# Performance work log

Measured on AMD Instinct MI355X. Metric: run time of the kernel, lower is better.

Reference implementation:

```python
import jax, jax.numpy as jnp
import numpy as np

B, N, C, OC, K = 8, 1024, 64, 64, 4


def setup_inputs() -> dict:
    key = jax.random.key(0)
    ks = jax.random.split(key, 10)
    stdv = 1.0 / np.sqrt(OC)
    wr = jax.random.uniform(ks[4], (K + 1, C, OC), minval=-stdv, maxval=stdv)
    wi = jax.random.uniform(ks[5], (K + 1, C, OC), minval=-stdv, maxval=stdv)
    mag = jnp.sqrt(wr ** 2 + wi ** 2)
    wr, wi = wr / mag, wi / mag  # unit-magnitude complex weights (as in __init__)
    return {
        "X_real": jax.random.normal(ks[0], (B, N, C), dtype=jnp.float32),
        "X_imag": jax.random.normal(ks[1], (B, N, C), dtype=jnp.float32),
        "L_real": jax.random.normal(ks[2], (B, K + 1, N, N), dtype=jnp.float32) * 0.05,
        "L_imag": jax.random.normal(ks[3], (B, K + 1, N, N), dtype=jnp.float32) * 0.05,
        "w_real": wr.astype(jnp.float32),
        "w_imag": wi.astype(jnp.float32),
        "aw_real": jax.random.normal(ks[6], (2 * C,), dtype=jnp.float32) * 0.1,
        "aw_imag": jax.random.normal(ks[7], (2 * C,), dtype=jnp.float32) * 0.1,
        "ab_real": jnp.zeros((), jnp.float32),
        "ab_imag": jnp.zeros((), jnp.float32),
        "pa_real": jnp.float32(0.25),  # CPReLU slope (real part)
        "pa_imag": jnp.float32(0.25),  # CPReLU slope (imag part)
    }


def reference(X_real, X_imag, L_real, L_imag, w_real, w_imag,
              aw_real, aw_imag, ab_real, ab_imag, pa_real, pa_imag):
    Cin = X_real.shape[-1]
    # --- GAT-style complex attention score: CVLinear([x_i, x_j]) decomposed ---
    # score[b,i,j] = <x_i, w_src> + <x_j, w_dst> + bias (complex)
    ws_r, wd_r = aw_real[:Cin], aw_real[Cin:]
    ws_i, wd_i = aw_imag[:Cin], aw_imag[Cin:]
    src_r = X_real @ ws_r - X_imag @ ws_i   # [B,N]
    src_i = X_real @ ws_i + X_imag @ ws_r
    dst_r = X_real @ wd_r - X_imag @ wd_i
    dst_i = X_real @ wd_i + X_imag @ wd_r
    s_r = src_r[:, :, None] + dst_r[:, None, :] + ab_real  # [B,N,N]
    s_i = src_i[:, :, None] + dst_i[:, None, :] + ab_imag
    # CPReLU: PReLU applied separately to real/imag
    s_r = jnp.where(s_r >= 0, s_r, pa_real * s_r)
    s_i = jnp.where(s_i >= 0, s_i, pa_imag * s_i)
    # PhaseSoftMax(dim=1): softmax on magnitude, keep phase
    mag = jnp.sqrt(s_r ** 2 + s_i ** 2)
    sm = jax.nn.softmax(mag, axis=1)
    safe = jnp.where(mag == 0, 1.0, mag)
    a_r = sm * s_r / safe  # [B,N,N]
    a_i = sm * s_i / safe
    # --- modulate complex Laplacian (broadcast over K+1 axis) ---
    Lr = L_real * a_r[:, None] - L_imag * a_i[:, None]   # [B,K+1,N,N]
    Li = L_real * a_i[:, None] + L_imag * a_r[:, None]
    # --- faithful to einsum 'bijk,bqjp->bijp': sum last axis of L, broadcast j ---
    SLr = Lr.sum(-1)  # [B,K+1,N]
    SLi = Li.sum(-1)
    ein = lambda S, X, W: jnp.einsum('bkn,bnc,kco->bno', S, X, W)
    out_r = ein(SLr, X_real, w_real) - ein(SLi, X_imag, w_imag)  # [B,N,OC]
    out_i = ein(SLi, X_real, w_real) + ein(SLr, X_imag, w_imag)
    return out_r, out_i
```

## Files before the change

kernel.cpp:

```cpp
#include <hip/hip_runtime.h>

typedef unsigned short u16;
typedef unsigned int   u32;

__device__ __forceinline__ float b2f(u16 u){
  u32 x = ((u32)u) << 16;
  float f;
  __builtin_memcpy(&f, &x, 4);
  return f;
}
__device__ __forceinline__ float ld(const void* p, int i, bool f32){
  return f32 ? ((const float*)p)[i] : b2f(((const u16*)p)[i]);
}

__global__ __launch_bounds__(256) void k_detect(
    const u16* __restrict__ X, const u16* __restrict__ L,
    const u16* __restrict__ w, const u16* __restrict__ aw,
    const u16* __restrict__ pa, float* __restrict__ flags)
{
  const int tid  = threadIdx.x;
  const int g    = tid >> 6;
  const int lane = tid & 63;
  const u16* src = (g == 0) ? X : (g == 1) ? L : (g == 2) ? w : aw;
  float v = fabsf(b2f(src[lane]));
  if (!(v < 1e30f)) v = 1e30f;
#pragma unroll
  for (int off = 32; off; off >>= 1){
    float o = __shfl_xor(v, off);
    v = v > o ? v : o;
  }
  if (lane == 0) flags[g] = (v > 1e6f) ? 1.f : 0.f;
  if (tid == 0)  flags[4] = (b2f(pa[0]) == 0.f) ? 1.f : 0.f;
}

__global__ __launch_bounds__(256) void k_srcdst(
    const void* __restrict__ Xr, const void* __restrict__ Xi,
    const void* __restrict__ awr, const void* __restrict__ awi,
    float* __restrict__ src_r, float* __restrict__ src_i,
    float* __restrict__ dst_r, float* __restrict__ dst_i,
    float* __restrict__ denom, const float* __restrict__ flags)
{
  const int tid = threadIdx.x;
  if (blockIdx.x < 32) denom[blockIdx.x * 256 + tid] = 0.f;

  const bool fX  = flags[0] != 0.f;
  const bool fAW = flags[3] != 0.f;

  const int bn = blockIdx.x * 4 + (tid >> 6);
  const int c  = tid & 63;
  float xr = ld(Xr, bn * 64 + c, fX);
  float xi = ld(Xi, bn * 64 + c, fX);
  float wsr = ld(awr, c, fAW),      wsi = ld(awi, c, fAW);
  float wdr = ld(awr, 64 + c, fAW), wdi = ld(awi, 64 + c, fAW);

  float p0 = xr * wsr - xi * wsi;
  float p1 = xr * wsi + xi * wsr;
  float p2 = xr * wdr - xi * wdi;
  float p3 = xr * wdi + xi * wdr;
#pragma unroll
  for (int off = 32; off; off >>= 1){
    p0 += __shfl_xor(p0, off);
    p1 += __shfl_xor(p1, off);
    p2 += __shfl_xor(p2, off);
    p3 += __shfl_xor(p3, off);
  }
  if (c == 0){
    src_r[bn] = p0; src_i[bn] = p1; dst_r[bn] = p2; dst_i[bn] = p3;
  }
}

__global__ __launch_bounds__(256) void k_colsum(
    const float* __restrict__ src_r, const float* __restrict__ src_i,
    const float* __restrict__ dst_r, const float* __restrict__ dst_i,
    const void* __restrict__ abr_p, const void* __restrict__ abi_p,
    const void* __restrict__ par_p, const void* __restrict__ pai_p,
    float* __restrict__ denom, const float* __restrict__ flags)
{
  __shared__ float srs[128], sis[128];
  const int tid = threadIdx.x;
  const int b  = blockIdx.x >> 5;
  const int mc = (blockIdx.x >> 3) & 3;
  const int nc = blockIdx.x & 7;
  const int m  = mc * 256 + tid;

  const bool fS = flags[4] != 0.f;
  const float abr = ld(abr_p, 0, fS), abi = ld(abi_p, 0, fS);
  const float par = ld(par_p, 0, fS), pai = ld(pai_p, 0, fS);

  if (tid < 128) srs[tid] = src_r[b * 1024 + nc * 128 + tid];
  else           sis[tid - 128] = src_i[b * 1024 + nc * 128 + (tid - 128)];
  __syncthreads();

  const float dr = dst_r[b * 1024 + m];
  const float di = dst_i[b * 1024 + m];
  float sum = 0.f;
#pragma unroll 4
  for (int j = 0; j < 128; j++){
    float sr = srs[j] + dr + abr; sr = sr >= 0.f ? sr : par * sr;
    float si = sis[j] + di + abi; si = si >= 0.f ? si : pai * si;
    float mag = sqrtf(sr * sr + si * si);
    sum += __expf(mag);
  }
  atomicAdd(&denom[b * 1024 + m], sum);
}

__global__ __launch_bounds__(256) void k_rowsum(
    const void* __restrict__ Lr, const void* __restrict__ Li,
    const float* __restrict__ src_r, const float* __restrict__ src_i,
    const float* __restrict__ dst_r, const float* __restrict__ dst_i,
    const float* __restrict__ denom,
    const void* __restrict__ abr_p, const void* __restrict__ abi_p,
    const void* __restrict__ par_p, const void* __restrict__ pai_p,
    float* __restrict__ SL, const float* __restrict__ flags)
{
  const int tid = threadIdx.x;
  const int bn  = blockIdx.x;
  const int b   = bn >> 10;
  const int n   = bn & 1023;

  const bool fL = flags[1] != 0.f;
  const bool fS = flags[4] != 0.f;

  const int base = b * 5 * 262144 + n * 256 + tid;
  float lr[5][4], li[5][4];
  if (fL){
    const float4* LrP = (const float4*)Lr;
    const float4* LiP = (const float4*)Li;
#pragma unroll
    for (int k = 0; k < 5; k++){
      float4 a = LrP[base + k * 262144];
      float4 c = LiP[base + k * 262144];
      lr[k][0]=a.x; lr[k][1]=a.y; lr[k][2]=a.z; lr[k][3]=a.w;
      li[k][0]=c.x; li[k][1]=c.y; li[k][2]=c.z; li[k][3]=c.w;
    }
  } else {
    const ushort4* LrP = (const ushort4*)Lr;
    const ushort4* LiP = (const ushort4*)Li;
#pragma unroll
    for (int k = 0; k < 5; k++){
      ushort4 a = LrP[base + k * 262144];
      ushort4 c = LiP[base + k * 262144];
      lr[k][0]=b2f(a.x); lr[k][1]=b2f(a.y); lr[k][2]=b2f(a.z); lr[k][3]=b2f(a.w);
      li[k][0]=b2f(c.x); li[k][1]=b2f(c.y); li[k][2]=b2f(c.z); li[k][3]=b2f(c.w);
    }
  }

  const int mb = b * 1024 + tid * 4;
  float4 dr4 = *(const float4*)(dst_r + mb);
  float4 di4 = *(const float4*)(dst_i + mb);
  float4 de4 = *(const float4*)(denom + mb);
  const float sR = src_r[bn], sI = src_i[bn];
  const float abr = ld(abr_p, 0, fS), abi = ld(abi_p, 0, fS);
  const float par = ld(par_p, 0, fS), pai = ld(pai_p, 0, fS);

  float drv[4], dvv[4], dev[4];
  *(float4*)drv = dr4; *(float4*)dvv = di4; *(float4*)dev = de4;

  float ar[4], ai[4];
#pragma unroll
  for (int j = 0; j < 4; j++){
    float sr = sR + drv[j] + abr; sr = sr >= 0.f ? sr : par * sr;
    float si = sI + dvv[j] + abi; si = si >= 0.f ? si : pai * si;
    float mag = sqrtf(sr * sr + si * si);
    float e = __expf(mag);
    float safe = mag > 0.f ? mag : 1.f;
    float coef = e / (dev[j] * safe);
    ar[j] = coef * sr;
    ai[j] = coef * si;
  }

  float v[10];
#pragma unroll
  for (int k = 0; k < 5; k++){
    float accr = 0.f, acci = 0.f;
#pragma unroll
    for (int j = 0; j < 4; j++){
      accr += lr[k][j] * ar[j] - li[k][j] * ai[j];
      acci += lr[k][j] * ai[j] + li[k][j] * ar[j];
    }
    v[k]     = accr;
    v[5 + k] = acci;
  }

#pragma unroll
  for (int off = 32; off; off >>= 1){
#pragma unroll
    for (int t = 0; t < 10; t++) v[t] += __shfl_xor(v[t], off);
  }
  __shared__ float red[4][10];
  if ((tid & 63) == 0){
#pragma unroll
    for (int t = 0; t < 10; t++) red[tid >> 6][t] = v[t];
  }
  __syncthreads();
  if (tid < 10)
    SL[bn * 10 + tid] = red[0][tid] + red[1][tid] + red[2][tid] + red[3][tid];
}

__global__ __launch_bounds__(256) void k_out(
    const void* __restrict__ Xr, const void* __restrict__ Xi,
    const void* __restrict__ wr, const void* __restrict__ wi,
    const float* __restrict__ SL, float* __restrict__ out,
    const float* __restrict__ flags)
{
  __shared__ __align__(16) float Xr_s[16 * 68];
  __shared__ __align__(16) float Xi_s[16 * 68];
  __shared__ __align__(16) float wrT[64 * 68];
  __shared__ __align__(16) float wiT[64 * 68];
  __shared__ float SL_s[160];

  const int tid = threadIdx.x;
  const int R0  = blockIdx.x * 16;
  const bool fX = flags[0] != 0.f;
  const bool fW = flags[2] != 0.f;

#pragma unroll
  for (int e = 0; e < 4; e++){
    int idx = tid + 256 * e;
    int r = idx >> 6, c = idx & 63;
    Xr_s[r * 68 + c] = ld(Xr, R0 * 64 + idx, fX);
    Xi_s[r * 68 + c] = ld(Xi, R0 * 64 + idx, fX);
  }
  if (tid < 160) SL_s[tid] = SL[R0 * 10 + tid];

  const int r  = tid & 15;
  const int o4 = tid >> 4;
  float outr[4] = {0.f, 0.f, 0.f, 0.f};
  float outi[4] = {0.f, 0.f, 0.f, 0.f};

  for (int k = 0; k < 5; k++){
    __syncthreads();
#pragma unroll
    for (int e = 0; e < 16; e++){
      int idx = tid + 256 * e;
      int c = idx >> 6, o = idx & 63;
      wrT[o * 68 + c] = ld(wr, k * 4096 + idx, fW);
      wiT[o * 68 + c] = ld(wi, k * 4096 + idx, fW);
    }
    __syncthreads();

    float Dr[4] = {0.f, 0.f, 0.f, 0.f};
    float Di[4] = {0.f, 0.f, 0.f, 0.f};
#pragma unroll 4
    for (int c0 = 0; c0 < 64; c0 += 4){
      float4 xr = *(const float4*)(Xr_s + r * 68 + c0);
      float4 xi = *(const float4*)(Xi_s + r * 68 + c0);
#pragma unroll
      for (int oo = 0; oo < 4; oo++){
        int o = o4 * 4 + oo;
        float4 a  = *(const float4*)(wrT + o * 68 + c0);
        float4 bb = *(const float4*)(wiT + o * 68 + c0);
        Dr[oo] += xr.x * a.x  + xr.y * a.y  + xr.z * a.z  + xr.w * a.w;
        Di[oo] += xi.x * bb.x + xi.y * bb.y + xi.z * bb.z + xi.w * bb.w;
      }
    }
    const float slr = SL_s[r * 10 + k];
    const float sli = SL_s[r * 10 + 5 + k];
#pragma unroll
    for (int oo = 0; oo < 4; oo++){
      outr[oo] += slr * Dr[oo] - sli * Di[oo];
      outi[oo] += sli * Dr[oo] + slr * Di[oo];
    }
  }

  __syncthreads();
#pragma unroll
  for (int oo = 0; oo < 4; oo++){
    int o = o4 * 4 + oo;
    wrT[r * 68 + o] = outr[oo];
    wiT[r * 68 + o] = outi[oo];
  }
  __syncthreads();
  {
    int flat = tid * 4;
    int rr = flat >> 6, o0 = flat & 63;
    float4 vr = *(const float4*)(wrT + rr * 68 + o0);
    float4 vi = *(const float4*)(wiT + rr * 68 + o0);
    *(float4*)(out + (R0 + rr) * 64 + o0)          = vr;
    *(float4*)(out + 524288 + (R0 + rr) * 64 + o0) = vi;
  }
}

extern "C" void kernel_launch(void* const* d_in, const int* in_sizes, int n_in,
                              void* d_out, int out_size, void* d_ws, size_t ws_size,
                              hipStream_t stream)
{
  const void* Xr  = d_in[0];
  const void* Xi  = d_in[1];
  const void* Lr  = d_in[2];
  const void* Li  = d_in[3];
  const void* wrp = d_in[4];
  const void* wip = d_in[5];
  const void* awr = d_in[6];
  const void* awi = d_in[7];
  const void* abr = d_in[8];
  const void* abi = d_in[9];
  const void* par = d_in[10];
  const void* pai = d_in[11];
  float* out = (float*)d_out;

  float* ws    = (float*)d_ws;
  float* src_r = ws;
  float* src_i = ws + 8192;
  float* dst_r = ws + 16384;
  float* dst_i = ws + 24576;
  float* denom = ws + 32768;
  float* SL    = ws + 40960;
  float* flags = ws + 122880;

  k_detect<<<1, 256, 0, stream>>>((const u16*)Xr, (const u16*)Lr, (const u16*)wrp,
                                  (const u16*)awr, (const u16*)par, flags);
  k_srcdst<<<2048, 256, 0, stream>>>(Xr, Xi, awr, awi, src_r, src_i, dst_r, dst_i,
                                     denom, flags);
  k_colsum<<<256, 256, 0, stream>>>(src_r, src_i, dst_r, dst_i, abr, abi, par, pai,
                                    denom, flags);
  k_rowsum<<<8192, 256, 0, stream>>>(Lr, Li, src_r, src_i, dst_r, dst_i, denom,
                                     abr, abi, par, pai, SL, flags);
  k_out<<<512, 256, 0, stream>>>(Xr, Xi, wrp, wip, SL, out, flags);
}
```

Measured before the change: 454.0 us.

## Map one row per wavefront in rowsum with prefetch; vectorize k_out loads

k_rowsum now gives each wavefront its own (b,n) row. Each lane walks four column chunks, and in the bf16 path the next chunk's L and dst/denom data is double-buffered in registers. The cross-wave shared-memory reduction and __syncthreads are dropped, and the grid shrinks to 2048 blocks with a launch_bounds occupancy hint. It also swaps in fast sqrt/rcp intrinsics and vectorizes the X and weight loads in k_out. The aim is better latency hiding on the dominant L stream, in exchange for higher register pressure and slightly less precise math.

```diff
diff --git a/kernel.cpp b/kernel.cpp
--- a/kernel.cpp
+++ b/kernel.cpp
@@ -104,7 +104,7 @@
   atomicAdd(&denom[b * 1024 + m], sum);
 }
 
-__global__ __launch_bounds__(256) void k_rowsum(
+__global__ __launch_bounds__(256, 4) void k_rowsum(
     const void* __restrict__ Lr, const void* __restrict__ Li,
     const float* __restrict__ src_r, const float* __restrict__ src_i,
     const float* __restrict__ dst_r, const float* __restrict__ dst_i,
@@ -113,88 +113,131 @@
     const void* __restrict__ par_p, const void* __restrict__ pai_p,
     float* __restrict__ SL, const float* __restrict__ flags)
 {
-  const int tid = threadIdx.x;
-  const int bn  = blockIdx.x;
-  const int b   = bn >> 10;
-  const int n   = bn & 1023;
+  const int tid  = threadIdx.x;
+  const int lane = tid & 63;
+  const int bn   = blockIdx.x * 4 + (tid >> 6);
+  const int b    = bn >> 10;
+  const int n    = bn & 1023;
 
   const bool fL = flags[1] != 0.f;
   const bool fS = flags[4] != 0.f;
 
-  const int base = b * 5 * 262144 + n * 256 + tid;
-  float lr[5][4], li[5][4];
-  if (fL){
-    const float4* LrP = (const float4*)Lr;
-    const float4* LiP = (const float4*)Li;
-#pragma unroll
-    for (int k = 0; k < 5; k++){
-      float4 a = LrP[base + k * 262144];
-      float4 c = LiP[base + k * 262144];
-      lr[k][0]=a.x; lr[k][1]=a.y; lr[k][2]=a.z; lr[k][3]=a.w;
-      li[k][0]=c.x; li[k][1]=c.y; li[k][2]=c.z; li[k][3]=c.w;
-    }
-  } else {
-    const ushort4* LrP = (const ushort4*)Lr;
-    const ushort4* LiP = (const ushort4*)Li;
-#pragma unroll
-    for (int k = 0; k < 5; k++){
-      ushort4 a = LrP[base + k * 262144];
-      ushort4 c = LiP[base + k * 262144];
-      lr[k][0]=b2f(a.x); lr[k][1]=b2f(a.y); lr[k][2]=b2f(a.z); lr[k][3]=b2f(a.w);
-      li[k][0]=b2f(c.x); li[k][1]=b2f(c.y); li[k][2]=b2f(c.z); li[k][3]=b2f(c.w);
-    }
-  }
-
-  const int mb = b * 1024 + tid * 4;
-  float4 dr4 = *(const float4*)(dst_r + mb);
-  float4 di4 = *(const float4*)(dst_i + mb);
-  float4 de4 = *(const float4*)(denom + mb);
   const float sR = src_r[bn], sI = src_i[bn];
   const float abr = ld(abr_p, 0, fS), abi = ld(abi_p, 0, fS);
   const float par = ld(par_p, 0, fS), pai = ld(pai_p, 0, fS);
 
-  float drv[4], dvv[4], dev[4];
-  *(float4*)drv = dr4; *(float4*)dvv = di4; *(float4*)dev = de4;
-
-  float ar[4], ai[4];
-#pragma unroll
-  for (int j = 0; j < 4; j++){
-    float sr = sR + drv[j] + abr; sr = sr >= 0.f ? sr : par * sr;
-    float si = sI + dvv[j] + abi; si = si >= 0.f ? si : pai * si;
-    float mag = sqrtf(sr * sr + si * si);
-    float e = __expf(mag);
-    float safe = mag > 0.f ? mag : 1.f;
-    float coef = e / (dev[j] * safe);
-    ar[j] = coef * sr;
-    ai[j] = coef * si;
-  }
-
-  float v[10];
-#pragma unroll
-  for (int k = 0; k < 5; k++){
-    float accr = 0.f, acci = 0.f;
+  float acc[10];
+#pragma unroll
+  for (int t = 0; t < 10; t++) acc[t] = 0.f;
+
+  const int rowbase = (b * 5 * 1024 + n) * 256;
+  const int dbase   = b * 1024;
+
+  if (!fL){
+    const ushort4* LrP = (const ushort4*)Lr;
+    const ushort4* LiP = (const ushort4*)Li;
+    ushort4 lb[2][5], mb[2][5];
+    float4 dr4[2], di4[2], de4[2];
+#pragma unroll
+    for (int k = 0; k < 5; k++){
+      lb[0][k] = LrP[rowbase + k * 262144 + lane];
+      mb[0][k] = LiP[rowbase + k * 262144 + lane];
+    }
+    dr4[0] = *(const float4*)(dst_r + dbase + lane * 4);
+    di4[0] = *(const float4*)(dst_i + dbase + lane * 4);
+    de4[0] = *(const float4*)(denom + dbase + lane * 4);
+
 #pragma unroll
     for (int j = 0; j < 4; j++){
-      accr += lr[k][j] * ar[j] - li[k][j] * ai[j];
-      acci += lr[k][j] * ai[j] + li[k][j] * ar[j];
-    }
-    v[k]     = accr;
-    v[5 + k] = acci;
+      const int cur = j & 1, nxt = cur ^ 1;
+      if (j < 3){
+        const int voff = (j + 1) * 64 + lane;
+#pragma unroll
+        for (int k = 0; k < 5; k++){
+          lb[nxt][k] = LrP[rowbase + k * 262144 + voff];
+          mb[nxt][k] = LiP[rowbase + k * 262144 + voff];
+        }
+        dr4[nxt] = *(const float4*)(dst_r + dbase + voff * 4);
+        di4[nxt] = *(const float4*)(dst_i + dbase + voff * 4);
+        de4[nxt] = *(const float4*)(denom + dbase + voff * 4);
+      }
+      float drv[4] = {dr4[cur].x, dr4[cur].y, dr4[cur].z, dr4[cur].w};
+      float dvv[4] = {di4[cur].x, di4[cur].y, di4[cur].z, di4[cur].w};
+      float dev[4] = {de4[cur].x, de4[cur].y, de4[cur].z, de4[cur].w};
+      float ar[4], ai[4];
+#pragma unroll
+      for (int q = 0; q < 4; q++){
+        float sr = sR + drv[q] + abr; sr = sr >= 0.f ? sr : par * sr;
+        float si = sI + dvv[q] + abi; si = si >= 0.f ? si : pai * si;
+        float mag = __builtin_amdgcn_sqrtf(sr * sr + si * si);
+        float e = __expf(mag);
+        float safe = mag > 0.f ? mag : 1.f;
+        float coef = e * __builtin_amdgcn_rcpf(dev[q] * safe);
+        ar[q] = coef * sr;
+        ai[q] = coef * si;
+      }
+#pragma unroll
+      for (int k = 0; k < 5; k++){
+        float l0 = b2f(lb[cur][k].x), l1 = b2f(lb[cur][k].y);
+        float l2 = b2f(lb[cur][k].z), l3 = b2f(lb[cur][k].w);
+        float m0 = b2f(mb[cur][k].x), m1 = b2f(mb[cur][k].y);
+        float m2 = b2f(mb[cur][k].z), m3 = b2f(mb[cur][k].w);
+        float accr = acc[k], acci = acc[5 + k];
+        accr += l0 * ar[0] - m0 * ai[0];
+        accr += l1 * ar[1] - m1 * ai[1];
+        accr += l2 * ar[2] - m2 * ai[2];
+        accr += l3 * ar[3] - m3 * ai[3];
+        acci += l0 * ai[0] + m0 * ar[0];
+        acci += l1 * ai[1] + m1 * ar[1];
+        acci += l2 * ai[2] + m2 * ar[2];
+        acci += l3 * ai[3] + m3 * ar[3];
+        acc[k] = accr; acc[5 + k] = acci;
+      }
+    }
+  } else {
+    const float4* LrP = (const float4*)Lr;
+    const float4* LiP = (const float4*)Li;
+    for (int j = 0; j < 4; j++){
+      const int voff = j * 64 + lane;
+      float4 dr4 = *(const float4*)(dst_r + dbase + voff * 4);
+      float4 di4 = *(const float4*)(dst_i + dbase + voff * 4);
+      float4 de4 = *(const float4*)(denom + dbase + voff * 4);
+      float drv[4] = {dr4.x, dr4.y, dr4.z, dr4.w};
+      float dvv[4] = {di4.x, di4.y, di4.z, di4.w};
+      float dev[4] = {de4.x, de4.y, de4.z, de4.w};
+      float ar[4], ai[4];
+#pragma unroll
+      for (int q = 0; q < 4; q++){
+        float sr = sR + drv[q] + abr; sr = sr >= 0.f ? sr : par * sr;
+        float si = sI + dvv[q] + abi; si = si >= 0.f ? si : pai * si;
+        float mag = __builtin_amdgcn_sqrtf(sr * sr + si * si);
+        float e = __expf(mag);
+        float safe = mag > 0.f ? mag : 1.f;
+        float coef = e * __builtin_amdgcn_rcpf(dev[q] * safe);
+        ar[q] = coef * sr;
+        ai[q] = coef * si;
+      }
+#pragma unroll 1
+      for (int k = 0; k < 5; k++){
+        float4 a = LrP[rowbase + k * 262144 + voff];
+        float4 c = LiP[rowbase + k * 262144 + voff];
+        acc[k]     += a.x*ar[0] - c.x*ai[0] + a.y*ar[1] - c.y*ai[1]
+                    + a.z*ar[2] - c.z*ai[2] + a.w*ar[3] - c.w*ai[3];
+        acc[5 + k] += a.x*ai[0] + c.x*ar[0] + a.y*ai[1] + c.y*ar[1]
+                    + a.z*ai[2] + c.z*ar[2] + a.w*ai[3] + c.w*ar[3];
+      }
+    }
   }
 
 #pragma unroll
   for (int off = 32; off; off >>= 1){
 #pragma unroll
-    for (int t = 0; t < 10; t++) v[t] += __shfl_xor(v[t], off);
-  }
-  __shared__ float red[4][10];
-  if ((tid & 63) == 0){
-#pragma unroll
-    for (int t = 0; t < 10; t++) red[tid >> 6][t] = v[t];
-  }
-  __syncthreads();
-  if (tid < 10)
-    SL[bn * 10 + tid] = red[0][tid] + red[1][tid] + red[2][tid] + red[3][tid];
+    for (int t = 0; t < 10; t++) acc[t] += __shfl_xor(acc[t], off);
+  }
+  if (lane == 0){
+#pragma unroll
+    for (int t = 0; t < 10; t++) SL[bn * 10 + t] = acc[t];
+  }
 }
 
 __global__ __launch_bounds__(256) void k_out(
@@ -214,12 +257,18 @@
   const bool fX = flags[0] != 0.f;
   const bool fW = flags[2] != 0.f;
 
-#pragma unroll
-  for (int e = 0; e < 4; e++){
-    int idx = tid + 256 * e;
-    int r = idx >> 6, c = idx & 63;
-    Xr_s[r * 68 + c] = ld(Xr, R0 * 64 + idx, fX);
-    Xi_s[r * 68 + c] = ld(Xi, R0 * 64 + idx, fX);
+  {
+    int base = tid * 4;
+    int r = base >> 6, c = base & 63;
+    if (!fX){
+      ushort4 a = ((const ushort4*)Xr)[R0 * 16 + tid];
+      ushort4 bb = ((const ushort4*)Xi)[R0 * 16 + tid];
+      *(float4*)(Xr_s + r * 68 + c) = make_float4(b2f(a.x), b2f(a.y), b2f(a.z), b2f(a.w));
+      *(float4*)(Xi_s + r * 68 + c) = make_float4(b2f(bb.x), b2f(bb.y), b2f(bb.z), b2f(bb.w));
+    } else {
+      *(float4*)(Xr_s + r * 68 + c) = ((const float4*)Xr)[R0 * 16 + tid];
+      *(float4*)(Xi_s + r * 68 + c) = ((const float4*)Xi)[R0 * 16 + tid];
+    }
   }
   if (tid < 160) SL_s[tid] = SL[R0 * 10 + tid];
 
@@ -231,11 +280,26 @@
   for (int k = 0; k < 5; k++){
     __syncthreads();
 #pragma unroll
-    for (int e = 0; e < 16; e++){
-      int idx = tid + 256 * e;
-      int c = idx >> 6, o = idx & 63;
-      wrT[o * 68 + c] = ld(wr, k * 4096 + idx, fW);
-      wiT[o * 68 + c] = ld(wi, k * 4096 + idx, fW);
+    for (int e = 0; e < 4; e++){
+      int vidx = tid + 256 * e;
+      int base = vidx * 4;
+      int c = base >> 6, o = base & 63;
+      float w0r, w1r, w2r, w3r, w0i, w1i, w2i, w3i;
+      if (!fW){
+        ushort4 a = ((const ushort4*)wr)[k * 1024 + vidx];
+        ushort4 bb = ((const ushort4*)wi)[k * 1024 + vidx];
+        w0r = b2f(a.x); w1r = b2f(a.y); w2r = b2f(a.z); w3r = b2f(a.w);
+        w0i = b2f(bb.x); w1i = b2f(bb.y); w2i = b2f(bb.z); w3i = b2f(bb.w);
+      } else {
+        float4 a = ((const float4*)wr)[k * 1024 + vidx];
+        float4 bb = ((const float4*)wi)[k * 1024 + vidx];
+        w0r = a.x; w1r = a.y; w2r = a.z; w3r = a.w;
+        w0i = bb.x; w1i = bb.y; w2i = bb.z; w3i = bb.w;
+      }
+      wrT[(o + 0) * 68 + c] = w0r; wrT[(o + 1) * 68 + c] = w1r;
+      wrT[(o + 2) * 68 + c] = w2r; wrT[(o + 3) * 68 + c] = w3r;
+      wiT[(o + 0) * 68 + c] = w0i; wiT[(o + 1) * 68 + c] = w1i;
+      wiT[(o + 2) * 68 + c] = w2i; wiT[(o + 3) * 68 + c] = w3i;
     }
     __syncthreads();
 
@@ -314,7 +378,7 @@
                                      denom, flags);
   k_colsum<<<256, 256, 0, stream>>>(src_r, src_i, dst_r, dst_i, abr, abi, par, pai,
                                     denom, flags);
-  k_rowsum<<<8192, 256, 0, stream>>>(Lr, Li, src_r, src_i, dst_r, dst_i, denom,
+  k_rowsum<<<2048, 256, 0, stream>>>(Lr, Li, src_r, src_i, dst_r, dst_i, denom,
                                      abr, abi, par, pai, SL, flags);
   k_out<<<512, 256, 0, stream>>>(Xr, Xi, wrp, wip, SL, out, flags);
 }
```

After: 424.7 us. 6.5% less time.
